# Kernel optimization log

Hardware: AMD Instinct MI355X
Metric: run time of the kernel (lower is better)

## Reference

```python
import jax, jax.numpy as jnp
import numpy as np
from jax import lax

EPS = 1e-5

def _conv(x, w, b, pad):
    y = lax.conv_general_dilated(x, w, (1, 1), [(pad, pad), (pad, pad)],
                                 dimension_numbers=('NCHW', 'OIHW', 'NCHW'))
    return y + b[None, :, None, None]

def _bn(x, g, b, m, v):
    # eval-mode BatchNorm2d with running stats
    scale = g * lax.rsqrt(v + EPS)
    return x * scale[None, :, None, None] + (b - m * scale)[None, :, None, None]

def setup_inputs() -> dict:
    key = jax.random.key(0)
    ks = jax.random.split(key, 16)
    B, C, H, W = 16, 64, 128, 128
    C2 = 2 * C
    d = {}
    d['x'] = jax.random.normal(ks[0], (B, C, H, W), jnp.float32)
    # fc1: Conv2d(C,C,3,p=1) + BN(C)
    d['fc1_w'] = jax.random.normal(ks[1], (C, C, 3, 3), jnp.float32) * 0.05
    d['fc1_b'] = jax.random.normal(ks[2], (C,), jnp.float32) * 0.05
    d['bn1_g'] = jnp.ones((C,), jnp.float32)
    d['bn1_b'] = jnp.zeros((C,), jnp.float32)
    d['bn1_m'] = jax.random.normal(ks[3], (C,), jnp.float32) * 0.05
    d['bn1_v'] = jax.random.uniform(ks[4], (C,), jnp.float32) * 0.5 + 0.5
    # graph_conv.nn: Conv2d(2C,2C,1) + BN(2C) + GELU
    d['gc_w'] = jax.random.normal(ks[5], (C2, C2, 1, 1), jnp.float32) * 0.05
    d['gc_b'] = jax.random.normal(ks[6], (C2,), jnp.float32) * 0.05
    d['bng_g'] = jnp.ones((C2,), jnp.float32)
    d['bng_b'] = jnp.zeros((C2,), jnp.float32)
    d['bng_m'] = jax.random.normal(ks[7], (C2,), jnp.float32) * 0.05
    d['bng_v'] = jax.random.uniform(ks[8], (C2,), jnp.float32) * 0.5 + 0.5
    # fc2: Conv2d(2C,C,3,p=1) + BN(C)
    d['fc2_w'] = jax.random.normal(ks[9], (C, C2, 3, 3), jnp.float32) * 0.05
    d['fc2_b'] = jax.random.normal(ks[10], (C,), jnp.float32) * 0.05
    d['bn2_g'] = jnp.ones((C,), jnp.float32)
    d['bn2_b'] = jnp.zeros((C,), jnp.float32)
    d['bn2_m'] = jax.random.normal(ks[11], (C,), jnp.float32) * 0.05
    d['bn2_v'] = jax.random.uniform(ks[12], (C,), jnp.float32) * 0.5 + 0.5
    return d

def reference(x, fc1_w, fc1_b, bn1_g, bn1_b, bn1_m, bn1_v,
              gc_w, gc_b, bng_g, bng_b, bng_m, bng_v,
              fc2_w, fc2_b, bn2_g, bn2_b, bn2_m, bn2_v):
    # fc1
    h = _bn(_conv(x, fc1_w, fc1_b, 1), bn1_g, bn1_b, bn1_m, bn1_v)
    # MRConv4dSP: strided self-attention over superpatch tokens
    sel = h[:, :, ::4, ::4]                          # [B,C,h4,w4]
    B, C, h4, w4 = sel.shape
    q = sel.reshape(B, C, h4 * w4).transpose(0, 2, 1)  # [B,N,C]
    scale = C ** (-0.5)
    att = jax.nn.softmax(jnp.einsum('bnc,bmc->bnm', q, q) * scale, axis=-1)
    o = jnp.einsum('bnm,bmc->bnc', att, q)           # [B,N,C]
    o = o.transpose(0, 2, 1).reshape(B, C, h4, w4)
    o = jnp.repeat(jnp.repeat(o, 4, axis=2), 4, axis=3)
    g = jnp.concatenate([h, o], axis=1)              # [B,2C,H,W]
    g = jax.nn.gelu(_bn(_conv(g, gc_w, gc_b, 0), bng_g, bng_b, bng_m, bng_v),
                    approximate=False)
    # fc2 + residual (drop_path=0 -> identity)
    y = _bn(_conv(g, fc2_w, fc2_b, 1), bn2_g, bn2_b, bn2_m, bn2_v)
    return y + x
```

## Files before the change

### kernel.cpp

```cpp
#include <hip/hip_runtime.h>
#include <math.h>

#define EPSV 1e-5f

typedef __bf16 bf16;
using bf16x8 = __attribute__((ext_vector_type(8))) __bf16;
using bf16x4 = __attribute__((ext_vector_type(4))) __bf16;
using bf16x2 = __attribute__((ext_vector_type(2))) __bf16;
using f32x4  = __attribute__((ext_vector_type(4))) float;

static __device__ __forceinline__ f32x4 mfma16(bf16x8 a, bf16x8 b, f32x4 c) {
    return __builtin_amdgcn_mfma_f32_16x16x32_bf16(a, b, c, 0, 0, 0);
}
static __device__ __forceinline__ f32x4 zero4() {
    f32x4 z = {0.f, 0.f, 0.f, 0.f};
    return z;
}

typedef __attribute__((address_space(1))) const char g_char_t;
typedef __attribute__((address_space(3))) char lds_char_t;
static __device__ __forceinline__ void gll16(const void* g, void* l) {
    __builtin_amdgcn_global_load_lds((g_char_t*)g, (lds_char_t*)l, 16, 0, 0);
}

static __device__ __forceinline__ float gelu_f(float v) {
    float z = fabsf(v) * 0.70710678118f;
    float t = __builtin_amdgcn_rcpf(1.f + 0.3275911f * z);
    float poly = t * (0.254829592f + t * (-0.284496736f + t * (1.421413741f +
                 t * (-1.453152027f + t * 1.061405429f))));
    float e = __expf(-z * z);
    float erfv = copysignf(1.f - poly * e, v);
    return 0.5f * v * (1.f + erfv);
}

template<int CIN>
__global__ __launch_bounds__(256) void prep_conv_w(const float* __restrict__ w,
                                                   bf16* __restrict__ wt)
{
    int t = blockIdx.x * 256 + threadIdx.x;
    if (t >= 64 * CIN) return;
    int cout = t / CIN, ci = t - cout * CIN;
    int cci = ci >> 5, lg = (ci >> 3) & 3, j = ci & 7;
#pragma unroll
    for (int kgt = 0; kgt < 9; ++kgt) {
        float v = w[(size_t)t * 9 + kgt];
        wt[((((size_t)kgt * (CIN >> 5) + cci) * 4 + lg) * 64 + cout) * 8 + j] = (bf16)v;
    }
}

__global__ __launch_bounds__(256) void prep_1x1_w(const float* __restrict__ w,
                                                  bf16* __restrict__ wt)
{
    int t = blockIdx.x * 256 + threadIdx.x;
    int cout = t >> 7, ci = t & 127;
    int ks = ci >> 5, lg = (ci >> 3) & 3, j = ci & 7;
    wt[(((size_t)(ks * 4 + lg) * 128) + cout) * 8 + j] = (bf16)w[t];
}

__global__ __launch_bounds__(256) void cvt_x_nhwc(const float* __restrict__ x,
                                                  bf16* __restrict__ xb,
                                                  float* __restrict__ zb)
{
    __shared__ float t_lds[64 * 68];
    const int bx = blockIdx.x;
    const int b  = blockIdx.y;
    const int y  = bx >> 1, x0 = (bx & 1) * 64;
    const int tid = threadIdx.x;

    if (bx == 0 && b == 0 && tid < 64)
        ((float4*)zb)[tid] = make_float4(0.f, 0.f, 0.f, 0.f);

    for (int f = tid; f < 64 * 16; f += 256) {
        int c = f >> 4, xu = f & 15;
        float4 v = *(const float4*)&x[((size_t)(b * 64 + c) << 14) + (y << 7) + x0 + xu * 4];
        t_lds[(xu * 4 + 0) * 68 + c] = v.x;
        t_lds[(xu * 4 + 1) * 68 + c] = v.y;
        t_lds[(xu * 4 + 2) * 68 + c] = v.z;
        t_lds[(xu * 4 + 3) * 68 + c] = v.w;
    }
    __syncthreads();
    for (int f = tid; f < 64 * 8; f += 256) {
        int xx = f >> 3, cu = f & 7;
        const float* p = &t_lds[xx * 68 + cu * 8];
        bf16x8 v;
#pragma unroll
        for (int j = 0; j < 8; ++j) v[j] = (bf16)p[j];
        *(bf16x8*)&xb[((size_t)((b * 128 + y) * 128) + x0 + xx) * 64 + cu * 8] = v;
    }
}

template<int CIN, int OUTMODE>
__global__ __launch_bounds__(256, 3) void conv3x3_mfma(
    const bf16* __restrict__ in, const bf16* __restrict__ wt,
    const float* __restrict__ bias,
    const float* __restrict__ bg, const float* __restrict__ bb,
    const float* __restrict__ bm, const float* __restrict__ bv,
    const bf16* __restrict__ resid, const bf16* __restrict__ zb,
    void* __restrict__ outp)
{
    constexpr int NC = CIN >> 5;
    __shared__ bf16 lds_all[2 * 12800];

    const int wg = blockIdx.x;
    const int v  = (wg & 7) * 128 + (wg >> 3);
    const int tile = v & 63, b = v >> 6;
    const int x0 = (tile & 1) * 64;
    const int y0 = (tile >> 1) * 4;
    const int tid  = threadIdx.x;
    const int wid  = tid >> 6;
    const int lane = tid & 63;
    const int lix  = lane & 15, lg = lane >> 4;
    const int nmine = (wid == 0) ? 7 : 6;

    int goff[7]; bool gok[7];
#pragma unroll
    for (int i = 0; i < 7; ++i) {
        int f = (wid + 4 * i) * 64 + lane;
        int pix = f >> 2, u = f & 3;
        int iy = pix / 66, ix = pix - iy * 66;
        int gy = y0 + iy - 1, gx = x0 + ix - 1;
        gok[i]  = (pix < 396) && (unsigned)gy < 128u && (unsigned)gx < 128u;
        goff[i] = ((b * 128 + gy) * 128 + gx) * CIN + u * 8;
    }
    int rd[9];
#pragma unroll
    for (int kg = 0; kg < 3; ++kg)
#pragma unroll
        for (int t = 0; t < 3; ++t)
            rd[kg * 3 + t] = ((wid + kg) * 66 + lix + t) * 32 + lg * 8;

    f32x4 acc[4][4];
#pragma unroll
    for (int i = 0; i < 4; ++i)
#pragma unroll
        for (int j = 0; j < 4; ++j) acc[i][j] = zero4();

    auto issue = [&](int cci, bf16* ldsbuf) {
#pragma unroll
        for (int i = 0; i < 7; ++i) {
            if (i < nmine) {
                const void* src = gok[i] ? (const void*)(in + goff[i] + cci * 32)
                                         : (const void*)zb;
                gll16(src, (char*)ldsbuf + (wid + 4 * i) * 1024);
            }
        }
    };
    auto load_af = [&](int kgt, int cci, bf16x8* af) {
        const bf16* wp = wt + ((((size_t)kgt * NC + cci) * 4 + lg) * 64) * 8;
#pragma unroll
        for (int mi = 0; mi < 4; ++mi)
            af[mi] = *(const bf16x8*)&wp[(mi * 16 + lix) * 8];
    };
    auto compute = [&](int cci, const bf16* buf) {
        bf16x8 afA[4], afB[4];
        load_af(0, cci, afA);
#pragma unroll
        for (int kgt = 0; kgt < 9; ++kgt) {
            bf16x8* cur = (kgt & 1) ? afB : afA;
            bf16x8* nxt = (kgt & 1) ? afA : afB;
            if (kgt < 8) load_af(kgt + 1, cci, nxt);
#pragma unroll
            for (int nj = 0; nj < 4; ++nj) {
                bf16x8 bfr = *(const bf16x8*)&buf[rd[kgt] + nj * 512];
#pragma unroll
                for (int mi = 0; mi < 4; ++mi)
                    acc[mi][nj] = mfma16(cur[mi], bfr, acc[mi][nj]);
            }
        }
    };

    bf16* ldsA = lds_all;
    bf16* ldsB = lds_all + 12800;
    issue(0, ldsA);
#pragma unroll 1
    for (int c = 0; c < NC; ++c) {
        const bf16* cur = (c & 1) ? ldsB : ldsA;
        bf16* nxt       = (c & 1) ? ldsA : ldsB;
        if (c + 1 < NC) {
            issue(c + 1, nxt);
            if (wid == 0) asm volatile("s_waitcnt vmcnt(7)" ::: "memory");
            else          asm volatile("s_waitcnt vmcnt(6)" ::: "memory");
        } else {
            asm volatile("s_waitcnt vmcnt(0)" ::: "memory");
        }
        __syncthreads();
        compute(c, cur);
        __syncthreads();
    }

    const int gy = y0 + wid;
    if (OUTMODE == 0) {
        bf16* stg = lds_all;
#pragma unroll
        for (int mi = 0; mi < 4; ++mi) {
            float A[4], Bc[4];
#pragma unroll
            for (int r = 0; r < 4; ++r) {
                int c = mi * 16 + lg * 4 + r;
                float s = bg[c] * rsqrtf(bv[c] + EPSV);
                A[r]  = s;
                Bc[r] = bias[c] * s + bb[c] - bm[c] * s;
            }
#pragma unroll
            for (int nj = 0; nj < 4; ++nj) {
                int px = nj * 16 + lix;
                bf16x4 vv;
#pragma unroll
                for (int r = 0; r < 4; ++r)
                    vv[r] = (bf16)(acc[mi][nj][r] * A[r] + Bc[r]);
                *(bf16x4*)&stg[(wid * 64 + px) * 64 + mi * 16 + lg * 4] = vv;
            }
        }
        __syncthreads();
        bf16* out = (bf16*)outp;
#pragma unroll
        for (int k = 0; k < 8; ++k) {
            int idx = k * 256 + tid;
            int row = idx >> 9, rem = idx & 511;
            int px = rem >> 3, cu = rem & 7;
            bf16x8 vv = *(const bf16x8*)&stg[(row * 64 + px) * 64 + cu * 8];
            *(bf16x8*)&out[((size_t)((b * 128 + y0 + row) * 128) + x0 + px) * 64 + cu * 8] = vv;
        }
    } else {
        float* out = (float*)outp;
#pragma unroll
        for (int mi = 0; mi < 4; ++mi) {
            float A[4], Bc[4];
#pragma unroll
            for (int r = 0; r < 4; ++r) {
                int c = mi * 16 + lg * 4 + r;
                float s = bg[c] * rsqrtf(bv[c] + EPSV);
                A[r]  = s;
                Bc[r] = bias[c] * s + bb[c] - bm[c] * s;
            }
#pragma unroll
            for (int nj = 0; nj < 4; ++nj) {
                int px = x0 + nj * 16 + lix;
                bf16x4 rv = *(const bf16x4*)&resid[((size_t)((b * 128 + gy) * 128) + px) * 64
                                                   + mi * 16 + lg * 4];
#pragma unroll
                for (int r = 0; r < 4; ++r) {
                    int c = mi * 16 + lg * 4 + r;
                    size_t oi = ((size_t)(b * 64 + c) << 14) + (gy << 7) + px;
                    out[oi] = acc[mi][nj][r] * A[r] + Bc[r] + (float)rv[r];
                }
            }
        }
    }
}

__global__ __launch_bounds__(256) void gather_q(const bf16* __restrict__ h,
                                                bf16* __restrict__ q)
{
    int t = blockIdx.x * 256 + threadIdx.x;
    int cu = t & 7, n = (t >> 3) & 1023, b = t >> 13;
    int y = (n >> 5) << 2, x = (n & 31) << 2;
    bf16x8 v = *(const bf16x8*)&h[((size_t)((b * 128 + y) * 128 + x)) * 64 + cu * 8];
    *(bf16x8*)&q[((size_t)(b * 1024 + n)) * 64 + cu * 8] = v;
}

__global__ __launch_bounds__(256) void attn_fused(const bf16* __restrict__ q,
                                                  bf16* __restrict__ o)
{
    __shared__ bf16 qn[64 * 72];
    __shared__ bf16 kn[128 * 72];
    __shared__ bf16 vt[64 * 136];
    __shared__ bf16 pl[4][16 * 136];
    __shared__ __align__(16) float fac[4][16];
    const int n0 = blockIdx.x * 64, b = blockIdx.y;
    const int tid = threadIdx.x, w = tid >> 6, lane = tid & 63;
    const int lix = lane & 15, lg = lane >> 4;
    const bf16* qb = q + ((size_t)b << 16);

    for (int f = tid; f < 512; f += 256) {
        int row = f >> 3, cu = f & 7;
        *(bf16x8*)&qn[row * 72 + cu * 8] =
            *(const bf16x8*)&qb[(size_t)(n0 + row) * 64 + cu * 8];
    }

    float m_run = -3.0e38f, l_run = 0.f;
    f32x4 oacc[4];
#pragma unroll
    for (int ct = 0; ct < 4; ++ct) oacc[ct] = zero4();

    for (int mt = 0; mt < 1024; mt += 128) {
        __syncthreads();
        for (int f = tid; f < 1024; f += 256) {
            int row = f >> 3, cu = f & 7;
            *(bf16x8*)&kn[row * 72 + cu * 8] =
                *(const bf16x8*)&qb[(size_t)(mt + row) * 64 + cu * 8];
        }
        for (int f = tid; f < 512; f += 256) {
            int mp = f >> 3, cu = f & 7;
            int m = mp * 2;
            bf16x8 a = *(const bf16x8*)&qb[(size_t)(mt + m) * 64 + cu * 8];
            bf16x8 c = *(const bf16x8*)&qb[(size_t)(mt + m + 1) * 64 + cu * 8];
#pragma unroll
            for (int j = 0; j < 8; ++j) {
                bf16x2 pr = {a[j], c[j]};
                *(bf16x2*)&vt[(cu * 8 + j) * 136 + m] = pr;
            }
        }
        __syncthreads();

        bf16x8 bq0 = *(const bf16x8*)&qn[(w * 16 + lix) * 72 + lg * 8];
        bf16x8 bq1 = *(const bf16x8*)&qn[(w * 16 + lix) * 72 + 32 + lg * 8];

        f32x4 s[8];
#pragma unroll
        for (int t = 0; t < 8; ++t) {
            bf16x8 a0 = *(const bf16x8*)&kn[(t * 16 + lix) * 72 + lg * 8];
            bf16x8 a1 = *(const bf16x8*)&kn[(t * 16 + lix) * 72 + 32 + lg * 8];
            s[t] = mfma16(a0, bq0, zero4());
            s[t] = mfma16(a1, bq1, s[t]);
        }

        float mx = -3.0e38f;
#pragma unroll
        for (int t = 0; t < 8; ++t)
#pragma unroll
            for (int r = 0; r < 4; ++r) { s[t][r] *= 0.125f; mx = fmaxf(mx, s[t][r]); }
        mx = fmaxf(mx, __shfl_xor(mx, 16));
        mx = fmaxf(mx, __shfl_xor(mx, 32));
        float m_new = fmaxf(m_run, mx);
        float alpha = __expf(m_run - m_new);

        float psum = 0.f;
#pragma unroll
        for (int t = 0; t < 8; ++t) {
            float p0 = __expf(s[t][0] - m_new), p1 = __expf(s[t][1] - m_new);
            float p2 = __expf(s[t][2] - m_new), p3 = __expf(s[t][3] - m_new);
            psum += (p0 + p1) + (p2 + p3);
            bf16x2 v01 = {(bf16)p0, (bf16)p1};
            bf16x2 v23 = {(bf16)p2, (bf16)p3};
            *(bf16x2*)&pl[w][lix * 136 + t * 16 + lg * 4]     = v01;
            *(bf16x2*)&pl[w][lix * 136 + t * 16 + lg * 4 + 2] = v23;
        }
        psum += __shfl_xor(psum, 16);
        psum += __shfl_xor(psum, 32);
        l_run = l_run * alpha + psum;
        m_run = m_new;
        if (lg == 0) fac[w][lix] = alpha;

        float4 a4 = *(const float4*)&fac[w][lg * 4];
        float aa[4] = {a4.x, a4.y, a4.z, a4.w};
#pragma unroll
        for (int ct = 0; ct < 4; ++ct)
#pragma unroll
            for (int r = 0; r < 4; ++r) oacc[ct][r] *= aa[r];

#pragma unroll
        for (int kk = 0; kk < 4; ++kk) {
            bf16x8 pa = *(const bf16x8*)&pl[w][lix * 136 + kk * 32 + lg * 8];
#pragma unroll
            for (int ct = 0; ct < 4; ++ct) {
                bf16x8 bv = *(const bf16x8*)&vt[(ct * 16 + lix) * 136 + kk * 32 + lg * 8];
                oacc[ct] = mfma16(pa, bv, oacc[ct]);
            }
        }
    }

    if (lg == 0) fac[w][lix] = l_run;
    float4 l4 = *(const float4*)&fac[w][lg * 4];
    float ll[4] = {1.f / l4.x, 1.f / l4.y, 1.f / l4.z, 1.f / l4.w};
#pragma unroll
    for (int ct = 0; ct < 4; ++ct)
#pragma unroll
        for (int r = 0; r < 4; ++r) {
            int n = n0 + w * 16 + lg * 4 + r;
            int c = ct * 16 + lix;
            o[((size_t)(b * 1024 + n)) * 64 + c] = (bf16)(oacc[ct][r] * ll[r]);
        }
}

__global__ __launch_bounds__(256) void conv1x1_mfma(
    const bf16* __restrict__ h, const bf16* __restrict__ ov,
    const bf16* __restrict__ wt, const float* __restrict__ bias,
    const float* __restrict__ bg, const float* __restrict__ bb,
    const float* __restrict__ bm, const float* __restrict__ bv,
    bf16* __restrict__ g)
{
    __shared__ bf16 in1[128 * 136];
    const int y = blockIdx.x, b = blockIdx.y;
    const int tid = threadIdx.x;
    const int wid = tid >> 6, lane = tid & 63;
    const int lix = lane & 15, lg = lane >> 4;
    const int wm = wid >> 1, wn = wid & 1;

    for (int f = tid; f < 128 * 16; f += 256) {
        int px = f >> 4, cu = f & 15;
        bf16x8 v;
        if (cu < 8) {
            v = *(const bf16x8*)&h[((size_t)((b * 128 + y) * 128 + px)) * 64 + cu * 8];
        } else {
            int n = ((y >> 2) << 5) + (px >> 2);
            v = *(const bf16x8*)&ov[((size_t)(b * 1024 + n)) * 64 + (cu - 8) * 8];
        }
        *(bf16x8*)&in1[px * 136 + cu * 8] = v;
    }
    __syncthreads();

    f32x4 acc[4][4];
#pragma unroll
    for (int i = 0; i < 4; ++i)
#pragma unroll
        for (int j = 0; j < 4; ++j) acc[i][j] = zero4();

#pragma unroll
    for (int ks = 0; ks < 4; ++ks) {
        bf16x8 af[4], bfv[4];
#pragma unroll
        for (int mi = 0; mi < 4; ++mi)
            af[mi] = *(const bf16x8*)&wt[(((size_t)(ks * 4 + lg) * 128) + wm * 64 + mi * 16 + lix) * 8];
#pragma unroll
        for (int nj = 0; nj < 4; ++nj)
            bfv[nj] = *(const bf16x8*)&in1[(wn * 64 + nj * 16 + lix) * 136 + ks * 32 + lg * 8];
#pragma unroll
        for (int mi = 0; mi < 4; ++mi)
#pragma unroll
            for (int nj = 0; nj < 4; ++nj)
                acc[mi][nj] = mfma16(af[mi], bfv[nj], acc[mi][nj]);
    }

    __syncthreads();
    bf16* stg = in1;
#pragma unroll
    for (int mi = 0; mi < 4; ++mi) {
        float A[4], Bc[4];
#pragma unroll
        for (int r = 0; r < 4; ++r) {
            int c = wm * 64 + mi * 16 + lg * 4 + r;
            float s = bg[c] * rsqrtf(bv[c] + EPSV);
            A[r]  = s;
            Bc[r] = bias[c] * s + bb[c] - bm[c] * s;
        }
#pragma unroll
        for (int nj = 0; nj < 4; ++nj) {
            int px = wn * 64 + nj * 16 + lix;
            bf16x4 vv;
#pragma unroll
            for (int r = 0; r < 4; ++r)
                vv[r] = (bf16)gelu_f(acc[mi][nj][r] * A[r] + Bc[r]);
            *(bf16x4*)&stg[px * 132 + wm * 64 + mi * 16 + lg * 4] = vv;
        }
    }
    __syncthreads();
#pragma unroll
    for (int k = 0; k < 8; ++k) {
        int idx = k * 256 + tid;
        int px = idx >> 4, cu = idx & 15;
        bf16x8 v = *(const bf16x8*)&stg[px * 132 + cu * 8];
        *(bf16x8*)&g[((size_t)((b * 128 + y) * 128) + px) * 128 + cu * 8] = v;
    }
}

extern "C" void kernel_launch(void* const* d_in, const int* in_sizes, int n_in,
                              void* d_out, int out_size, void* d_ws, size_t ws_size,
                              hipStream_t stream)
{
    const float* x     = (const float*)d_in[0];
    const float* fc1_w = (const float*)d_in[1];
    const float* fc1_b = (const float*)d_in[2];
    const float* bn1_g = (const float*)d_in[3];
    const float* bn1_b = (const float*)d_in[4];
    const float* bn1_m = (const float*)d_in[5];
    const float* bn1_v = (const float*)d_in[6];
    const float* gc_w  = (const float*)d_in[7];
    const float* gc_b  = (const float*)d_in[8];
    const float* bng_g = (const float*)d_in[9];
    const float* bng_b = (const float*)d_in[10];
    const float* bng_m = (const float*)d_in[11];
    const float* bng_v = (const float*)d_in[12];
    const float* fc2_w = (const float*)d_in[13];
    const float* fc2_b = (const float*)d_in[14];
    const float* bn2_g = (const float*)d_in[15];
    const float* bn2_b = (const float*)d_in[16];
    const float* bn2_m = (const float*)d_in[17];
    const float* bn2_v = (const float*)d_in[18];

    char* wsb = (char*)d_ws;
    bf16* x_bf = (bf16*)wsb;
    bf16* h    = (bf16*)(wsb + 33554432);
    bf16* g    = (bf16*)(wsb + 67108864);
    bf16* q    = (bf16*)(wsb + 134217728);
    bf16* o    = (bf16*)(wsb + 136314880);
    bf16* wt1  = (bf16*)(wsb + 138412032);
    bf16* wt2  = (bf16*)(wsb + 138485760);
    bf16* wtg  = (bf16*)(wsb + 138633216);
    bf16* zb   = (bf16*)(wsb + 138665984);

    prep_conv_w<64><<<16, 256, 0, stream>>>(fc1_w, wt1);
    prep_conv_w<128><<<32, 256, 0, stream>>>(fc2_w, wt2);
    prep_1x1_w<<<64, 256, 0, stream>>>(gc_w, wtg);

    cvt_x_nhwc<<<dim3(256, 16), 256, 0, stream>>>(x, x_bf, (float*)zb);

    conv3x3_mfma<64, 0><<<1024, 256, 0, stream>>>(
        x_bf, wt1, fc1_b, bn1_g, bn1_b, bn1_m, bn1_v, nullptr, zb, h);

    gather_q<<<512, 256, 0, stream>>>(h, q);

    attn_fused<<<dim3(16, 16), 256, 0, stream>>>(q, o);

    conv1x1_mfma<<<dim3(128, 16), 256, 0, stream>>>(
        h, o, wtg, gc_b, bng_g, bng_b, bng_m, bng_v, g);

    conv3x3_mfma<128, 1><<<1024, 256, 0, stream>>>(
        g, wt2, fc2_b, bn2_g, bn2_b, bn2_m, bn2_v, x_bf, zb, (float*)d_out);
}
```

Measured before the change: 189.1 us.

## Enlarge conv3x3 tiles to 8 rows with 512-thread blocks and single LDS buffer

The 3x3 conv kernel now uses 512-thread blocks, each covering an 8-row by 64-pixel tile instead of 4 rows, so the 1-row halo is amortised over more output rows and fewer blocks are launched. The double-buffered LDS input pipeline and the weight-fragment prefetch are replaced by one LDS buffer, with a full wait and barrier before each channel chunk. The bf16 epilogue stages output in two passes through a padded LDS layout. The cost is losing the overlap of global loads with MFMA compute, and possibly lower occupancy from the larger blocks.

```diff
diff --git a/kernel.cpp b/kernel.cpp
--- a/kernel.cpp
+++ b/kernel.cpp
@@ -90,7 +90,7 @@
 }
 
 template<int CIN, int OUTMODE>
-__global__ __launch_bounds__(256, 3) void conv3x3_mfma(
+__global__ __launch_bounds__(512) void conv3x3_mfma(
     const bf16* __restrict__ in, const bf16* __restrict__ wt,
     const float* __restrict__ bias,
     const float* __restrict__ bg, const float* __restrict__ bb,
@@ -99,27 +99,28 @@
     void* __restrict__ outp)
 {
     constexpr int NC = CIN >> 5;
-    __shared__ bf16 lds_all[2 * 12800];
+    __shared__ bf16 lds_buf[672 * 32];
 
     const int wg = blockIdx.x;
-    const int v  = (wg & 7) * 128 + (wg >> 3);
-    const int tile = v & 63, b = v >> 6;
+    const int v  = (wg & 7) * 64 + (wg >> 3);
+    const int tile = v & 31, b = v >> 5;
     const int x0 = (tile & 1) * 64;
-    const int y0 = (tile >> 1) * 4;
+    const int y0 = (tile >> 1) * 8;
     const int tid  = threadIdx.x;
     const int wid  = tid >> 6;
     const int lane = tid & 63;
     const int lix  = lane & 15, lg = lane >> 4;
-    const int nmine = (wid == 0) ? 7 : 6;
-
-    int goff[7]; bool gok[7];
-#pragma unroll
-    for (int i = 0; i < 7; ++i) {
-        int f = (wid + 4 * i) * 64 + lane;
+
+    int goff[6]; bool gok[6];
+#pragma unroll
+    for (int i = 0; i < 6; ++i) {
+        int chunk = wid + 8 * i;
+        int f = chunk * 64 + lane;
         int pix = f >> 2, u = f & 3;
         int iy = pix / 66, ix = pix - iy * 66;
         int gy = y0 + iy - 1, gx = x0 + ix - 1;
-        gok[i]  = (pix < 396) && (unsigned)gy < 128u && (unsigned)gx < 128u;
+        gok[i]  = (chunk < 42) && (pix < 660) &&
+                  (unsigned)gy < 128u && (unsigned)gx < 128u;
         goff[i] = ((b * 128 + gy) * 128 + gx) * CIN + u * 8;
     }
     int rd[9];
@@ -135,94 +136,90 @@
 #pragma unroll
         for (int j = 0; j < 4; ++j) acc[i][j] = zero4();
 
-    auto issue = [&](int cci, bf16* ldsbuf) {
-#pragma unroll
-        for (int i = 0; i < 7; ++i) {
-            if (i < nmine) {
+    auto issue = [&](int cci) {
+#pragma unroll
+        for (int i = 0; i < 6; ++i) {
+            int chunk = wid + 8 * i;
+            if (chunk < 42) {
                 const void* src = gok[i] ? (const void*)(in + goff[i] + cci * 32)
                                          : (const void*)zb;
-                gll16(src, (char*)ldsbuf + (wid + 4 * i) * 1024);
+                gll16(src, (char*)lds_buf + chunk * 1024);
             }
         }
     };
-    auto load_af = [&](int kgt, int cci, bf16x8* af) {
-        const bf16* wp = wt + ((((size_t)kgt * NC + cci) * 4 + lg) * 64) * 8;
-#pragma unroll
-        for (int mi = 0; mi < 4; ++mi)
-            af[mi] = *(const bf16x8*)&wp[(mi * 16 + lix) * 8];
+    auto compute = [&](int cci) {
+#pragma unroll
+        for (int kgt = 0; kgt < 9; ++kgt) {
+            bf16x8 af[4];
+            const bf16* wp = wt + ((((size_t)kgt * NC + cci) * 4 + lg) * 64) * 8;
+#pragma unroll
+            for (int mi = 0; mi < 4; ++mi)
+                af[mi] = *(const bf16x8*)&wp[(mi * 16 + lix) * 8];
+#pragma unroll
+            for (int nj = 0; nj < 4; ++nj) {
+                bf16x8 bfr = *(const bf16x8*)&lds_buf[rd[kgt] + nj * 512];
+#pragma unroll
+                for (int mi = 0; mi < 4; ++mi)
+                    acc[mi][nj] = mfma16(af[mi], bfr, acc[mi][nj]);
+            }
+        }
     };
-    auto compute = [&](int cci, const bf16* buf) {
-        bf16x8 afA[4], afB[4];
-        load_af(0, cci, afA);
-#pragma unroll
-        for (int kgt = 0; kgt < 9; ++kgt) {
-            bf16x8* cur = (kgt & 1) ? afB : afA;
-            bf16x8* nxt = (kgt & 1) ? afA : afB;
-            if (kgt < 8) load_af(kgt + 1, cci, nxt);
-#pragma unroll
-            for (int nj = 0; nj < 4; ++nj) {
-                bf16x8 bfr = *(const bf16x8*)&buf[rd[kgt] + nj * 512];
-#pragma unroll
-                for (int mi = 0; mi < 4; ++mi)
-                    acc[mi][nj] = mfma16(cur[mi], bfr, acc[mi][nj]);
-            }
-        }
-    };
-
-    bf16* ldsA = lds_all;
-    bf16* ldsB = lds_all + 12800;
-    issue(0, ldsA);
+
+    issue(0);
 #pragma unroll 1
     for (int c = 0; c < NC; ++c) {
-        const bf16* cur = (c & 1) ? ldsB : ldsA;
-        bf16* nxt       = (c & 1) ? ldsA : ldsB;
+        asm volatile("s_waitcnt vmcnt(0)" ::: "memory");
+        __syncthreads();
+        compute(c);
         if (c + 1 < NC) {
-            issue(c + 1, nxt);
-            if (wid == 0) asm volatile("s_waitcnt vmcnt(7)" ::: "memory");
-            else          asm volatile("s_waitcnt vmcnt(6)" ::: "memory");
-        } else {
-            asm volatile("s_waitcnt vmcnt(0)" ::: "memory");
-        }
-        __syncthreads();
-        compute(c, cur);
-        __syncthreads();
-    }
-
-    const int gy = y0 + wid;
+            __syncthreads();
+            issue(c + 1);
+        }
+    }
+
     if (OUTMODE == 0) {
-        bf16* stg = lds_all;
-#pragma unroll
-        for (int mi = 0; mi < 4; ++mi) {
-            float A[4], Bc[4];
-#pragma unroll
-            for (int r = 0; r < 4; ++r) {
-                int c = mi * 16 + lg * 4 + r;
-                float s = bg[c] * rsqrtf(bv[c] + EPSV);
-                A[r]  = s;
-                Bc[r] = bias[c] * s + bb[c] - bm[c] * s;
-            }
-#pragma unroll
-            for (int nj = 0; nj < 4; ++nj) {
-                int px = nj * 16 + lix;
-                bf16x4 vv;
-#pragma unroll
-                for (int r = 0; r < 4; ++r)
-                    vv[r] = (bf16)(acc[mi][nj][r] * A[r] + Bc[r]);
-                *(bf16x4*)&stg[(wid * 64 + px) * 64 + mi * 16 + lg * 4] = vv;
-            }
-        }
-        __syncthreads();
         bf16* out = (bf16*)outp;
-#pragma unroll
-        for (int k = 0; k < 8; ++k) {
-            int idx = k * 256 + tid;
-            int row = idx >> 9, rem = idx & 511;
-            int px = rem >> 3, cu = rem & 7;
-            bf16x8 vv = *(const bf16x8*)&stg[(row * 64 + px) * 64 + cu * 8];
-            *(bf16x8*)&out[((size_t)((b * 128 + y0 + row) * 128) + x0 + px) * 64 + cu * 8] = vv;
+        bf16* stg = lds_buf;
+#pragma unroll 1
+        for (int p = 0; p < 2; ++p) {
+            __syncthreads();
+            if ((wid >> 2) == p) {
+                int rl = wid & 3;
+#pragma unroll
+                for (int mi = 0; mi < 4; ++mi) {
+                    float A[4], Bc[4];
+#pragma unroll
+                    for (int r = 0; r < 4; ++r) {
+                        int c = mi * 16 + lg * 4 + r;
+                        float s = bg[c] * rsqrtf(bv[c] + EPSV);
+                        A[r]  = s;
+                        Bc[r] = bias[c] * s + bb[c] - bm[c] * s;
+                    }
+#pragma unroll
+                    for (int nj = 0; nj < 4; ++nj) {
+                        int px = nj * 16 + lix;
+                        bf16x4 vv;
+#pragma unroll
+                        for (int r = 0; r < 4; ++r)
+                            vv[r] = (bf16)(acc[mi][nj][r] * A[r] + Bc[r]);
+                        *(bf16x4*)&stg[(rl * 64 + px) * 68 + mi * 16 + lg * 4] = vv;
+                    }
+                }
+            }
+            __syncthreads();
+#pragma unroll
+            for (int k = 0; k < 4; ++k) {
+                int idx = k * 512 + tid;
+                int row = idx >> 9, rem = idx & 511;
+                int px = rem >> 3, cu = rem & 7;
+                bf16x8 vv = *(const bf16x8*)&stg[(row * 64 + px) * 68 + cu * 8];
+                *(bf16x8*)&out[((size_t)((b * 128 + y0 + p * 4 + row) * 128)
+                                + x0 + px) * 64 + cu * 8] = vv;
+            }
         }
     } else {
         float* out = (float*)outp;
+        const int gy = y0 + wid;
 #pragma unroll
         for (int mi = 0; mi < 4; ++mi) {
             float A[4], Bc[4];
@@ -495,7 +492,7 @@
 
     cvt_x_nhwc<<<dim3(256, 16), 256, 0, stream>>>(x, x_bf, (float*)zb);
 
-    conv3x3_mfma<64, 0><<<1024, 256, 0, stream>>>(
+    conv3x3_mfma<64, 0><<<512, 512, 0, stream>>>(
         x_bf, wt1, fc1_b, bn1_g, bn1_b, bn1_m, bn1_v, nullptr, zb, h);
 
     gather_q<<<512, 256, 0, stream>>>(h, q);
@@ -505,6 +502,6 @@
     conv1x1_mfma<<<dim3(128, 16), 256, 0, stream>>>(
         h, o, wtg, gc_b, bng_g, bng_b, bng_m, bng_v, g);
 
-    conv3x3_mfma<128, 1><<<1024, 256, 0, stream>>>(
+    conv3x3_mfma<128, 1><<<512, 512, 0, stream>>>(
         g, wt2, fc2_b, bn2_g, bn2_b, bn2_m, bn2_v, x_bf, zb, (float*)d_out);
 }
```

Result: slower. 195.8 us (+3.5%).
